# Kernel tuning notes

Hardware: AMD Instinct MI355X
Metric: run time of the kernel (lower is better)

The kernel has to match this reference:

```python
import math
import jax, jax.numpy as jnp
import numpy as np

B, L, D, H = 4, 512, 256, 8
DH = D // H
BUCKETS = 11  # rel_pos_buckets; padding_idx = BUCKETS


def setup_inputs() -> dict:
    key = jax.random.key(0)
    ks = jax.random.split(key, 12)
    s = 0.02
    rel_table = jax.random.normal(ks[10], (BUCKETS + 1, D), dtype=jnp.float32) * s
    rel_table = rel_table.at[BUCKETS].set(0.0)  # padding_idx row is zero
    return {
        "inputs": jax.random.normal(ks[0], (B, L, D), dtype=jnp.float32),
        "mask": jax.random.randint(ks[1], (B, L, L), 0, 2) > 0,
        "distances": jax.random.randint(ks[2], (B, L, L), 0, BUCKETS + 1),
        "Wq": jax.random.normal(ks[3], (D, D), dtype=jnp.float32) * s,
        "bq": jnp.zeros((D,), jnp.float32),
        "Wk": jax.random.normal(ks[4], (D, D), dtype=jnp.float32) * s,
        "bk": jnp.zeros((D,), jnp.float32),
        "Wv": jax.random.normal(ks[5], (D, D), dtype=jnp.float32) * s,
        "bv": jnp.zeros((D,), jnp.float32),
        "Wo": jax.random.normal(ks[6], (D, D), dtype=jnp.float32) * s,
        "bo": jnp.zeros((D,), jnp.float32),
        "rel_table": rel_table,
        "u": jax.random.normal(ks[7], (D,), dtype=jnp.float32) * s,
        "v": jax.random.normal(ks[8], (D,), dtype=jnp.float32) * s,
    }


def reference(inputs, mask, distances, Wq, bq, Wk, bk, Wv, bv, Wo, bo, rel_table, u, v):
    def shape(x):  # (B, L, D) -> (B, H, L, DH)
        return x.reshape(B, L, H, DH).transpose(0, 2, 1, 3)

    q = shape(inputs @ Wq + bq) / math.sqrt(DH)
    k = shape(inputs @ Wk + bk)
    val = shape(inputs @ Wv + bv)

    # content term: (q + u) k^T
    a_c = jnp.einsum("bhqd,bhkd->bhqk", q + u.reshape(1, H, 1, DH), k)

    # relative-position term: embedding gather (padding row already zero, mask anyway)
    valid = (distances != BUCKETS)[..., None].astype(rel_table.dtype)
    rel = (rel_table[distances] * valid).reshape(B, L, L, H, DH)  # (B, Lq, Lk, H, DH)
    b_d = jnp.einsum("bhqd,bqkhd->bhqk", q + v.reshape(1, H, 1, DH), rel)

    scores = jnp.where(mask[:, None, :, :], jnp.float32(-1e18), a_c + b_d)
    attn = jax.nn.softmax(scores, axis=-1)  # (B, H, Lq, Lk)

    ctx = jnp.einsum("bhqk,bhkd->bhqd", attn, val)
    ctx = ctx.transpose(0, 2, 1, 3).reshape(B, L, D)
    output = ctx @ Wo + bo
    return output, attn
```

## Files before the change

### kernel.cpp

```cpp
#include <hip/hip_runtime.h>
#include <math.h>

#define BB 4
#define LL 512
#define DD 256
#define HH 8
#define DHH 32
#define NB 12

__global__ __launch_bounds__(256) void qkv_kernel(const float* __restrict__ x,
    const float* __restrict__ Wq, const float* __restrict__ bq,
    const float* __restrict__ Wk, const float* __restrict__ bk,
    const float* __restrict__ Wv, const float* __restrict__ bv,
    float* __restrict__ Q, float* __restrict__ K, float* __restrict__ V) {
    __shared__ float xs[8][DD];
    const int mat = blockIdx.x >> 8;
    const int r0 = (blockIdx.x & 255) * 8;
    const int c = threadIdx.x;
    const float* W;
    const float* bias;
    float* dst;
    float scale;
    if (mat == 0)      { W = Wq; bias = bq; dst = Q; scale = 0.17677669529663687f; }
    else if (mat == 1) { W = Wk; bias = bk; dst = K; scale = 1.0f; }
    else               { W = Wv; bias = bv; dst = V; scale = 1.0f; }
#pragma unroll
    for (int r = 0; r < 8; ++r) xs[r][c] = x[(r0 + r) * DD + c];
    __syncthreads();
    float acc[8];
#pragma unroll
    for (int r = 0; r < 8; ++r) acc[r] = bias[c];
    for (int i = 0; i < DD; ++i) {
        const float wv = W[i * DD + c];
#pragma unroll
        for (int r = 0; r < 8; ++r) acc[r] = fmaf(xs[r][i], wv, acc[r]);
    }
#pragma unroll
    for (int r = 0; r < 8; ++r) dst[(r0 + r) * DD + c] = acc[r] * scale;
}

__global__ __launch_bounds__(512) void scores_kernel(const float* __restrict__ Q,
    const float* __restrict__ Km, const float* __restrict__ uvec,
    const float* __restrict__ vvec, const float* __restrict__ rel_table,
    const int* __restrict__ mask, const int* __restrict__ dist,
    float* __restrict__ attn) {
    __shared__ float Qu[8][DHH];
    __shared__ float Qv8[8][DHH];
    __shared__ float rels[NB][DHH + 1];
    __shared__ float Ps[8][NB];
    __shared__ float wsum[8][8];
    const int blk = blockIdx.x;
    const int h = blk & 7;
    const int rest = blk >> 3;
    const int qt = rest & 63;
    const int b = rest >> 6;
    const int q0 = qt * 8;
    const int t = threadIdx.x;
    const int w = t >> 6, l = t & 63;

    if (t < 256) {
        const int r = t >> 5, c = t & 31;
        const float qv = Q[(b * LL + q0 + r) * DD + h * DHH + c];
        Qu[r][c]  = qv + uvec[h * DHH + c];
        Qv8[r][c] = qv + vvec[h * DHH + c];
    }
    if (t < NB * DHH) {
        rels[t >> 5][t & 31] = rel_table[(t >> 5) * DD + h * DHH + (t & 31)];
    }
    __syncthreads();
    if (t < 8 * NB) {
        const int bk = t >> 3, r = t & 7;
        float a = 0.f;
#pragma unroll
        for (int d = 0; d < DHH; ++d) a = fmaf(Qv8[r][d], rels[bk][d], a);
        Ps[r][bk] = a;
    }
    __syncthreads();

    float4 kr[8];
    const float4* kp = (const float4*)&Km[(b * LL + t) * DD + h * DHH];
#pragma unroll
    for (int j = 0; j < 8; ++j) kr[j] = kp[j];

    float e[8];
#pragma unroll
    for (int r = 0; r < 8; ++r) {
        const int mq = (b * LL + q0 + r) * LL + t;
        float acc = Ps[r][dist[mq]];
#pragma unroll
        for (int j = 0; j < 8; ++j) {
            acc = fmaf(Qu[r][4 * j + 0], kr[j].x, acc);
            acc = fmaf(Qu[r][4 * j + 1], kr[j].y, acc);
            acc = fmaf(Qu[r][4 * j + 2], kr[j].z, acc);
            acc = fmaf(Qu[r][4 * j + 3], kr[j].w, acc);
        }
        e[r] = mask[mq] ? 0.f : __expf(acc);
    }

    float sm[8];
#pragma unroll
    for (int r = 0; r < 8; ++r) {
        float s = e[r];
        for (int off = 32; off > 0; off >>= 1) s += __shfl_xor(s, off);
        sm[r] = s;
    }
    if (l == 0) {
#pragma unroll
        for (int r = 0; r < 8; ++r) wsum[r][w] = sm[r];
    }
    __syncthreads();
#pragma unroll
    for (int r = 0; r < 8; ++r) {
        float tot = wsum[r][0];
#pragma unroll
        for (int i = 1; i < 8; ++i) tot += wsum[r][i];
        attn[((long)(b * HH + h) * LL + q0 + r) * LL + t] = e[r] * (1.0f / tot);
    }
}

__global__ __launch_bounds__(256) void ctx_out_kernel(const float* __restrict__ attn,
    const float* __restrict__ V, const float* __restrict__ Wo,
    const float* __restrict__ bo, float* __restrict__ out) {
    __shared__ float Cs[4][DD];
    const int blk = blockIdx.x;
    const int b = blk >> 7;
    const int q0 = (blk & 127) * 4;
    const int d = threadIdx.x;
    const int h = d >> 5;
    const float* vb = V + b * LL * DD + d;
    const float* ab = attn + ((long)(b * HH + h) * LL + q0) * LL;
    float acc[4] = {0.f, 0.f, 0.f, 0.f};
    for (int k0 = 0; k0 < LL; k0 += 4) {
        const float v0 = vb[(k0 + 0) * DD];
        const float v1 = vb[(k0 + 1) * DD];
        const float v2 = vb[(k0 + 2) * DD];
        const float v3 = vb[(k0 + 3) * DD];
#pragma unroll
        for (int q = 0; q < 4; ++q) {
            const float4 a = *(const float4*)&ab[q * LL + k0];
            acc[q] = fmaf(a.x, v0, fmaf(a.y, v1, fmaf(a.z, v2, fmaf(a.w, v3, acc[q]))));
        }
    }
#pragma unroll
    for (int q = 0; q < 4; ++q) Cs[q][d] = acc[q];
    __syncthreads();
    float o[4];
#pragma unroll
    for (int q = 0; q < 4; ++q) o[q] = bo[d];
    for (int i = 0; i < DD; ++i) {
        const float wv = Wo[i * DD + d];
#pragma unroll
        for (int q = 0; q < 4; ++q) o[q] = fmaf(Cs[q][i], wv, o[q]);
    }
#pragma unroll
    for (int q = 0; q < 4; ++q) out[(b * LL + q0 + q) * DD + d] = o[q];
}

extern "C" void kernel_launch(void* const* d_in, const int* in_sizes, int n_in,
                              void* d_out, int out_size, void* d_ws, size_t ws_size,
                              hipStream_t stream) {
    const float* x    = (const float*)d_in[0];
    const int* mk     = (const int*)d_in[1];
    const int* dist   = (const int*)d_in[2];
    const float* Wq = (const float*)d_in[3];
    const float* bq = (const float*)d_in[4];
    const float* Wk = (const float*)d_in[5];
    const float* bk = (const float*)d_in[6];
    const float* Wv = (const float*)d_in[7];
    const float* bv = (const float*)d_in[8];
    const float* Wo = (const float*)d_in[9];
    const float* bo = (const float*)d_in[10];
    const float* rel_table = (const float*)d_in[11];
    const float* uvec = (const float*)d_in[12];
    const float* vvec = (const float*)d_in[13];

    float* out  = (float*)d_out;
    float* attn = out + BB * LL * DD;

    float* Q = (float*)d_ws;
    float* K = Q + BB * LL * DD;
    float* V = K + BB * LL * DD;

    qkv_kernel<<<3 * 256, 256, 0, stream>>>(x, Wq, bq, Wk, bk, Wv, bv, Q, K, V);
    scores_kernel<<<BB * (LL / 8) * HH, 512, 0, stream>>>(Q, K, uvec, vvec, rel_table,
                                                          mk, dist, attn);
    ctx_out_kernel<<<BB * (LL / 4), 256, 0, stream>>>(attn, V, Wo, bo, out);
}
```

Baseline: 193.3 us.

## Store V transposed and vectorize loads across QKV, scores and ctx kernels

The QKV kernel now writes V transposed per batch (d-major) so the ctx kernel can read V with float4 loads along the key dimension, and it loads the x tile into shared memory with float4. The scores kernel hoists the dist and mask loads ahead of the dot products and reads Qu as float4. The ctx kernel splits the accumulation into two chains over eight keys per step and reads Cs as float4 in the Wo projection. In exchange, the transposed V stores are strided per thread (each thread writes 8 contiguous floats at a 2 KB stride) and register pressure rises.

```diff
diff --git a/kernel.cpp b/kernel.cpp
--- a/kernel.cpp
+++ b/kernel.cpp
@@ -12,20 +12,22 @@
     const float* __restrict__ Wq, const float* __restrict__ bq,
     const float* __restrict__ Wk, const float* __restrict__ bk,
     const float* __restrict__ Wv, const float* __restrict__ bv,
-    float* __restrict__ Q, float* __restrict__ K, float* __restrict__ V) {
+    float* __restrict__ Q, float* __restrict__ K, float* __restrict__ VT) {
     __shared__ float xs[8][DD];
     const int mat = blockIdx.x >> 8;
     const int r0 = (blockIdx.x & 255) * 8;
     const int c = threadIdx.x;
     const float* W;
     const float* bias;
-    float* dst;
-    float scale;
-    if (mat == 0)      { W = Wq; bias = bq; dst = Q; scale = 0.17677669529663687f; }
-    else if (mat == 1) { W = Wk; bias = bk; dst = K; scale = 1.0f; }
-    else               { W = Wv; bias = bv; dst = V; scale = 1.0f; }
-#pragma unroll
-    for (int r = 0; r < 8; ++r) xs[r][c] = x[(r0 + r) * DD + c];
+    if (mat == 0)      { W = Wq; bias = bq; }
+    else if (mat == 1) { W = Wk; bias = bk; }
+    else               { W = Wv; bias = bv; }
+    {
+        float4* xsv = (float4*)&xs[0][0];
+        const float4* xg = (const float4*)&x[r0 * DD];
+        xsv[c] = xg[c];
+        xsv[c + 256] = xg[c + 256];
+    }
     __syncthreads();
     float acc[8];
 #pragma unroll
@@ -35,8 +37,20 @@
 #pragma unroll
         for (int r = 0; r < 8; ++r) acc[r] = fmaf(xs[r][i], wv, acc[r]);
     }
-#pragma unroll
-    for (int r = 0; r < 8; ++r) dst[(r0 + r) * DD + c] = acc[r] * scale;
+    if (mat == 0) {
+#pragma unroll
+        for (int r = 0; r < 8; ++r)
+            Q[(r0 + r) * DD + c] = acc[r] * 0.17677669529663687f;
+    } else if (mat == 1) {
+#pragma unroll
+        for (int r = 0; r < 8; ++r) K[(r0 + r) * DD + c] = acc[r];
+    } else {
+        const int b = r0 >> 9;
+        const int lk = r0 & 511;
+        float* vtp = VT + ((long)(b * DD + c)) * LL + lk;
+#pragma unroll
+        for (int r = 0; r < 8; ++r) vtp[r] = acc[r];
+    }
 }
 
 __global__ __launch_bounds__(512) void scores_kernel(const float* __restrict__ Q,
@@ -82,19 +96,28 @@
 #pragma unroll
     for (int j = 0; j < 8; ++j) kr[j] = kp[j];
 
+    int dv[8], mv[8];
+#pragma unroll
+    for (int r = 0; r < 8; ++r) {
+        const int mq = (b * LL + q0 + r) * LL + t;
+        dv[r] = dist[mq];
+        mv[r] = mask[mq];
+    }
+
     float e[8];
 #pragma unroll
     for (int r = 0; r < 8; ++r) {
-        const int mq = (b * LL + q0 + r) * LL + t;
-        float acc = Ps[r][dist[mq]];
+        float acc = Ps[r][dv[r]];
+        const float4* qup = (const float4*)&Qu[r][0];
 #pragma unroll
         for (int j = 0; j < 8; ++j) {
-            acc = fmaf(Qu[r][4 * j + 0], kr[j].x, acc);
-            acc = fmaf(Qu[r][4 * j + 1], kr[j].y, acc);
-            acc = fmaf(Qu[r][4 * j + 2], kr[j].z, acc);
-            acc = fmaf(Qu[r][4 * j + 3], kr[j].w, acc);
+            const float4 qq = qup[j];
+            acc = fmaf(qq.x, kr[j].x, acc);
+            acc = fmaf(qq.y, kr[j].y, acc);
+            acc = fmaf(qq.z, kr[j].z, acc);
+            acc = fmaf(qq.w, kr[j].w, acc);
         }
-        e[r] = mask[mq] ? 0.f : __expf(acc);
+        e[r] = mv[r] ? 0.f : __expf(acc);
     }
 
     float sm[8];
@@ -119,7 +142,7 @@
 }
 
 __global__ __launch_bounds__(256) void ctx_out_kernel(const float* __restrict__ attn,
-    const float* __restrict__ V, const float* __restrict__ Wo,
+    const float* __restrict__ VT, const float* __restrict__ Wo,
     const float* __restrict__ bo, float* __restrict__ out) {
     __shared__ float Cs[4][DD];
     const int blk = blockIdx.x;
@@ -127,30 +150,37 @@
     const int q0 = (blk & 127) * 4;
     const int d = threadIdx.x;
     const int h = d >> 5;
-    const float* vb = V + b * LL * DD + d;
+    const float* vt = VT + ((long)(b * DD + d)) * LL;
     const float* ab = attn + ((long)(b * HH + h) * LL + q0) * LL;
-    float acc[4] = {0.f, 0.f, 0.f, 0.f};
-    for (int k0 = 0; k0 < LL; k0 += 4) {
-        const float v0 = vb[(k0 + 0) * DD];
-        const float v1 = vb[(k0 + 1) * DD];
-        const float v2 = vb[(k0 + 2) * DD];
-        const float v3 = vb[(k0 + 3) * DD];
+    float accA[4] = {0.f, 0.f, 0.f, 0.f};
+    float accB[4] = {0.f, 0.f, 0.f, 0.f};
+    for (int k0 = 0; k0 < LL; k0 += 8) {
+        const float4 v0 = *(const float4*)&vt[k0];
+        const float4 v1 = *(const float4*)&vt[k0 + 4];
 #pragma unroll
         for (int q = 0; q < 4; ++q) {
-            const float4 a = *(const float4*)&ab[q * LL + k0];
-            acc[q] = fmaf(a.x, v0, fmaf(a.y, v1, fmaf(a.z, v2, fmaf(a.w, v3, acc[q]))));
+            const float4 a0 = *(const float4*)&ab[q * LL + k0];
+            const float4 a1 = *(const float4*)&ab[q * LL + k0 + 4];
+            accA[q] = fmaf(a0.x, v0.x, fmaf(a0.y, v0.y, fmaf(a0.z, v0.z, fmaf(a0.w, v0.w, accA[q]))));
+            accB[q] = fmaf(a1.x, v1.x, fmaf(a1.y, v1.y, fmaf(a1.z, v1.z, fmaf(a1.w, v1.w, accB[q]))));
         }
     }
 #pragma unroll
-    for (int q = 0; q < 4; ++q) Cs[q][d] = acc[q];
+    for (int q = 0; q < 4; ++q) Cs[q][d] = accA[q] + accB[q];
     __syncthreads();
     float o[4];
 #pragma unroll
     for (int q = 0; q < 4; ++q) o[q] = bo[d];
-    for (int i = 0; i < DD; ++i) {
-        const float wv = Wo[i * DD + d];
-#pragma unroll
-        for (int q = 0; q < 4; ++q) o[q] = fmaf(Cs[q][i], wv, o[q]);
+    for (int i = 0; i < DD; i += 4) {
+        const float w0 = Wo[(i + 0) * DD + d];
+        const float w1 = Wo[(i + 1) * DD + d];
+        const float w2 = Wo[(i + 2) * DD + d];
+        const float w3 = Wo[(i + 3) * DD + d];
+#pragma unroll
+        for (int q = 0; q < 4; ++q) {
+            const float4 cv = *(const float4*)&Cs[q][i];
+            o[q] = fmaf(cv.x, w0, fmaf(cv.y, w1, fmaf(cv.z, w2, fmaf(cv.w, w3, o[q]))));
+        }
     }
 #pragma unroll
     for (int q = 0; q < 4; ++q) out[(b * LL + q0 + q) * DD + d] = o[q];
@@ -177,12 +207,12 @@
     float* out  = (float*)d_out;
     float* attn = out + BB * LL * DD;
 
-    float* Q = (float*)d_ws;
-    float* K = Q + BB * LL * DD;
-    float* V = K + BB * LL * DD;
-
-    qkv_kernel<<<3 * 256, 256, 0, stream>>>(x, Wq, bq, Wk, bk, Wv, bv, Q, K, V);
+    float* Q  = (float*)d_ws;
+    float* K  = Q + BB * LL * DD;
+    float* VT = K + BB * LL * DD;
+
+    qkv_kernel<<<3 * 256, 256, 0, stream>>>(x, Wq, bq, Wk, bk, Wv, bv, Q, K, VT);
     scores_kernel<<<BB * (LL / 8) * HH, 512, 0, stream>>>(Q, K, uvec, vvec, rel_table,
                                                           mk, dist, attn);
-    ctx_out_kernel<<<BB * (LL / 4), 256, 0, stream>>>(attn, V, Wo, bo, out);
-}
+    ctx_out_kernel<<<BB * (LL / 4), 256, 0, stream>>>(attn, VT, Wo, bo, out);
+}
```

After: 212.9 us. 10.1% more time.
